# Kernel optimization log

Measured on AMD Instinct MI355X. Metric: run time of the kernel, lower is better.

## Reference

```python
import jax, jax.numpy as jnp
import numpy as np

N = 8192
D_IN, D_GAT, D_GCN = 128, 64, 64


def setup_inputs() -> dict:
    key = jax.random.key(0)
    ks = jax.random.split(key, 7)
    feat = jax.random.normal(ks[0], (N, D_IN), dtype=jnp.float32)
    r = jax.random.uniform(ks[1], (N, N), dtype=jnp.float32)
    sup = jnp.where(r < 0.01, r * 100.0, 0.0)
    xav = lambda k, shape: jax.random.normal(k, shape, dtype=jnp.float32) * jnp.sqrt(2.0 / (shape[0] + shape[1]))
    W_map = xav(ks[2], (D_IN, D_GAT))
    b_map = jnp.zeros((1,), dtype=jnp.float32)
    U = xav(ks[3], (D_GAT, 1))
    V = xav(ks[4], (D_GAT, 1))
    W_gcn = xav(ks[5], (D_GAT, D_GCN))
    return {"feat": feat, "sup": sup, "W_map": W_map, "b_map": b_map, "U": U, "V": V, "W_gcn": W_gcn}


def reference(feat, sup, W_map, b_map, U, V, W_gcn):
    n = sup.shape[0]
    sup2 = sup + jnp.eye(n, dtype=sup.dtype)  # add self-loops
    # GAT layer
    h = feat @ W_map                            # [N, D_GAT]
    s = h @ U                                   # [N, 1] score from source node i
    t = h @ V                                   # [N, 1] score from target node j
    # torch loop builds att[j, i] = tanh(s_i + t_j + b)
    att = jnp.tanh(s.T + t + b_map)             # [N, N]
    att = jnp.where(sup2 > 0, att, jnp.float32(-100.0))
    att = jax.nn.softmax(att, axis=1)
    gat_feat = jnp.tanh(att @ h)                # [N, D_GAT]
    # GCN layer (dropout is identity at inference)
    agg = sup2 @ gat_feat                       # [N, D_GAT]
    out = jax.nn.relu(agg @ W_gcn)              # [N, D_GCN]
    norm = jnp.linalg.norm(out, axis=1, keepdims=True)
    out = out / jnp.maximum(norm, jnp.float32(1e-12))  # F.normalize(p=2, dim=1)
    return out
```

## Files before the change

kernel.cpp:

```cpp
#include <hip/hip_runtime.h>
#include <hip/hip_bf16.h>


#define N_NODES 8192
#define D_IN    128
#define D_GAT   64
#define SLOTS   256

__global__ __launch_bounds__(256) void k1_map(
    const float* __restrict__ feat, const float* __restrict__ W_map,
    const float* __restrict__ U, const float* __restrict__ V,
    float* __restrict__ h, float* __restrict__ s, float* __restrict__ t)
{
    const int r = threadIdx.x >> 6;
    const int d = threadIdx.x & 63;
    const int row = blockIdx.x * 4 + r;
    __shared__ float f[4 * D_IN];
    if (threadIdx.x < 128)
        ((float4*)f)[threadIdx.x] =
            ((const float4*)(feat + (size_t)blockIdx.x * 4 * D_IN))[threadIdx.x];
    __syncthreads();

    const float* fr = f + r * D_IN;
    float acc = 0.f;
#pragma unroll 8
    for (int k = 0; k < D_IN; ++k)
        acc += fr[k] * W_map[k * D_GAT + d];
    h[row * D_GAT + d] = acc;

    float sv = acc * U[d];
    float tv = acc * V[d];
#pragma unroll
    for (int off = 32; off > 0; off >>= 1) {
        sv += __shfl_xor(sv, off);
        tv += __shfl_xor(tv, off);
    }
    if (d == 0) { s[row] = sv; t[row] = tv; }
}

__global__ __launch_bounds__(256) void k2_compact(
    const float* __restrict__ sup,
    int* __restrict__ cnt, int* __restrict__ col, float* __restrict__ val)
{
    const int j = blockIdx.x;
    const int lane = threadIdx.x & 63;
    __shared__ int c;
    if (threadIdx.x == 0) c = 0;
    __syncthreads();
    const float4* row = (const float4*)(sup + (size_t)j * N_NODES);
    int*   colj = col + j * SLOTS;
    float* valj = val + j * SLOTS;

    for (int q = threadIdx.x; q < N_NODES / 4; q += 256) {
        float4 v = row[q];
        const int i0 = q * 4;
        float vs[4] = {v.x, v.y, v.z, v.w};
#pragma unroll
        for (int u = 0; u < 4; ++u) {
            const int i = i0 + u;
            const float vv = vs[u] + ((i == j) ? 1.0f : 0.0f);
            const bool keep = vv > 0.f;
            const unsigned long long mask = __ballot(keep);
            if (mask) {
                int base = 0;
                if (lane == 0) base = atomicAdd(&c, __popcll(mask));
                base = __shfl(base, 0);
                if (keep) {
                    const int pos = base +
                        __popcll(mask & ((1ull << lane) - 1ull));
                    if (pos < SLOTS) { colj[pos] = i; valj[pos] = vv; }
                }
            }
        }
    }
    __syncthreads();
    if (threadIdx.x == 0) cnt[j] = (c < SLOTS) ? c : SLOTS;
}

__global__ __launch_bounds__(64) void k3_gat(
    const float* __restrict__ h, const float* __restrict__ s,
    const float* __restrict__ t, const float* __restrict__ b,
    const int* __restrict__ cnt, const int* __restrict__ col,
    float* __restrict__ gat)
{
    const int j = blockIdx.x;
    const int lane = threadIdx.x;
    const int m = cnt[j];
    const int* colj = col + j * SLOTS;
    __shared__ int   cl[SLOTS];
    __shared__ float w[SLOTS];
    const float tj = t[j] + b[0];

    float lmax = -1e30f;
    for (int p = lane; p < m; p += 64) {
        const int ci = colj[p];
        cl[p] = ci;
        const float e = tanhf(s[ci] + tj);
        w[p] = e;
        lmax = fmaxf(lmax, e);
    }
#pragma unroll
    for (int off = 32; off > 0; off >>= 1)
        lmax = fmaxf(lmax, __shfl_xor(lmax, off));

    float lsum = 0.f;
    for (int p = lane; p < m; p += 64) {
        const float e = __expf(w[p] - lmax);
        w[p] = e;
        lsum += e;
    }
#pragma unroll
    for (int off = 32; off > 0; off >>= 1) lsum += __shfl_xor(lsum, off);
    __syncthreads();

    const int c16 = (lane & 15) * 4;
    const int pp  = lane >> 4;
    float4 acc = make_float4(0.f, 0.f, 0.f, 0.f);
    for (int base = 0; base < m; base += 4) {
        const int p = base + pp;
        if (p < m) {
            const float wp = w[p];
            const float4 hv = *(const float4*)(h + cl[p] * D_GAT + c16);
            acc.x += wp * hv.x; acc.y += wp * hv.y;
            acc.z += wp * hv.z; acc.w += wp * hv.w;
        }
    }
#pragma unroll
    for (int off = 16; off <= 32; off <<= 1) {
        acc.x += __shfl_xor(acc.x, off); acc.y += __shfl_xor(acc.y, off);
        acc.z += __shfl_xor(acc.z, off); acc.w += __shfl_xor(acc.w, off);
    }
    if (pp == 0) {
        const float inv = 1.0f / lsum;
        float4 o;
        o.x = tanhf(acc.x * inv); o.y = tanhf(acc.y * inv);
        o.z = tanhf(acc.z * inv); o.w = tanhf(acc.w * inv);
        *(float4*)(gat + j * D_GAT + c16) = o;
    }
}

__global__ __launch_bounds__(64) void k4_gcn(
    const float* __restrict__ gat, const float* __restrict__ W_gcn,
    const int* __restrict__ cnt, const int* __restrict__ col,
    const float* __restrict__ val, float* __restrict__ out)
{
    const int j = blockIdx.x;
    const int lane = threadIdx.x;
    const int m = cnt[j];
    const int*   colj = col + j * SLOTS;
    const float* valj = val + j * SLOTS;
    __shared__ int   cl[SLOTS];
    __shared__ float wv[SLOTS];
    for (int p = lane; p < m; p += 64) { cl[p] = colj[p]; wv[p] = valj[p]; }
    __syncthreads();

    const int c16 = (lane & 15) * 4;
    const int pp  = lane >> 4;
    float4 acc = make_float4(0.f, 0.f, 0.f, 0.f);
    for (int base = 0; base < m; base += 4) {
        const int p = base + pp;
        if (p < m) {
            const float wp = wv[p];
            const float4 gv = *(const float4*)(gat + cl[p] * D_GAT + c16);
            acc.x += wp * gv.x; acc.y += wp * gv.y;
            acc.z += wp * gv.z; acc.w += wp * gv.w;
        }
    }
#pragma unroll
    for (int off = 16; off <= 32; off <<= 1) {
        acc.x += __shfl_xor(acc.x, off); acc.y += __shfl_xor(acc.y, off);
        acc.z += __shfl_xor(acc.z, off); acc.w += __shfl_xor(acc.w, off);
    }
    __shared__ float a[D_GAT];
    if (pp == 0) *(float4*)(a + c16) = acc;
    __syncthreads();

    float o = 0.f;
#pragma unroll 8
    for (int d = 0; d < D_GAT; ++d)
        o += a[d] * W_gcn[d * D_GAT + lane];
    o = fmaxf(o, 0.f);

    float ss = o * o;
#pragma unroll
    for (int off = 32; off > 0; off >>= 1) ss += __shfl_xor(ss, off);
    const float nrm = sqrtf(ss);
    out[j * D_GAT + lane] = o / fmaxf(nrm, 1e-12f);
}

extern "C" void kernel_launch(void* const* d_in, const int* in_sizes, int n_in,
                              void* d_out, int out_size, void* d_ws, size_t ws_size,
                              hipStream_t stream) {
    const float* feat  = (const float*)d_in[0];
    const float* sup   = (const float*)d_in[1];
    const float* W_map = (const float*)d_in[2];
    const float* b_map = (const float*)d_in[3];
    const float* U     = (const float*)d_in[4];
    const float* V     = (const float*)d_in[5];
    const float* W_gcn = (const float*)d_in[6];
    float* out = (float*)d_out;

    char* ws = (char*)d_ws;
    float* h   = (float*)(ws);
    float* gat = (float*)(ws + (2u << 20));
    float* s   = (float*)(ws + (4u << 20));
    float* t   = (float*)(ws + (4u << 20) + 32768);
    int*   cnt = (int*)  (ws + (4u << 20) + 65536);
    int*   col = (int*)  (ws + (4u << 20) + 98304);
    float* val = (float*)(ws + (12u << 20) + 98304);

    k1_map    <<<N_NODES / 4, 256, 0, stream>>>(feat, W_map, U, V, h, s, t);
    k2_compact<<<N_NODES,     256, 0, stream>>>(sup, cnt, col, val);
    k3_gat    <<<N_NODES,      64, 0, stream>>>(h, s, t, b_map, cnt, col, gat);
    k4_gcn    <<<N_NODES,      64, 0, stream>>>(gat, W_gcn, cnt, col, val, out);
}
```

Baseline: 412.1 us.

## Merge map and compaction kernels; pack four rows per block in gather kernels

Combines the feature-mapping kernel and the adjacency compaction kernel into a single launch, split by block index, which removes one launch and lets the two independent phases run concurrently. The GAT and GCN gather kernels now process four rows per 256-thread block, each wave using its own shared-memory slices. Their gather loops are unrolled by four with separate accumulators to keep more independent loads in flight. The total run is dominated by the compaction, which streams the dense 256 MB adjacency matrix, so these changes mostly trim overheads around that cost. Shared-memory use per block rises, and the block-wide barriers now couple four rows.

```diff
diff --git a/kernel.cpp b/kernel.cpp
--- a/kernel.cpp
+++ b/kernel.cpp
@@ -6,89 +6,89 @@
 #define D_IN    128
 #define D_GAT   64
 #define SLOTS   256
-
-__global__ __launch_bounds__(256) void k1_map(
+#define K1_BLOCKS (N_NODES / 4)
+
+__global__ __launch_bounds__(256) void k12_map_compact(
     const float* __restrict__ feat, const float* __restrict__ W_map,
     const float* __restrict__ U, const float* __restrict__ V,
-    float* __restrict__ h, float* __restrict__ s, float* __restrict__ t)
-{
-    const int r = threadIdx.x >> 6;
-    const int d = threadIdx.x & 63;
-    const int row = blockIdx.x * 4 + r;
-    __shared__ float f[4 * D_IN];
-    if (threadIdx.x < 128)
-        ((float4*)f)[threadIdx.x] =
-            ((const float4*)(feat + (size_t)blockIdx.x * 4 * D_IN))[threadIdx.x];
-    __syncthreads();
-
-    const float* fr = f + r * D_IN;
-    float acc = 0.f;
-#pragma unroll 8
-    for (int k = 0; k < D_IN; ++k)
-        acc += fr[k] * W_map[k * D_GAT + d];
-    h[row * D_GAT + d] = acc;
-
-    float sv = acc * U[d];
-    float tv = acc * V[d];
-#pragma unroll
-    for (int off = 32; off > 0; off >>= 1) {
-        sv += __shfl_xor(sv, off);
-        tv += __shfl_xor(tv, off);
-    }
-    if (d == 0) { s[row] = sv; t[row] = tv; }
-}
-
-__global__ __launch_bounds__(256) void k2_compact(
     const float* __restrict__ sup,
+    float* __restrict__ h, float* __restrict__ s, float* __restrict__ t,
     int* __restrict__ cnt, int* __restrict__ col, float* __restrict__ val)
 {
-    const int j = blockIdx.x;
-    const int lane = threadIdx.x & 63;
-    __shared__ int c;
-    if (threadIdx.x == 0) c = 0;
-    __syncthreads();
-    const float4* row = (const float4*)(sup + (size_t)j * N_NODES);
-    int*   colj = col + j * SLOTS;
-    float* valj = val + j * SLOTS;
-
-    for (int q = threadIdx.x; q < N_NODES / 4; q += 256) {
-        float4 v = row[q];
-        const int i0 = q * 4;
-        float vs[4] = {v.x, v.y, v.z, v.w};
-#pragma unroll
-        for (int u = 0; u < 4; ++u) {
-            const int i = i0 + u;
-            const float vv = vs[u] + ((i == j) ? 1.0f : 0.0f);
-            const bool keep = vv > 0.f;
-            const unsigned long long mask = __ballot(keep);
-            if (mask) {
-                int base = 0;
-                if (lane == 0) base = atomicAdd(&c, __popcll(mask));
-                base = __shfl(base, 0);
-                if (keep) {
-                    const int pos = base +
-                        __popcll(mask & ((1ull << lane) - 1ull));
-                    if (pos < SLOTS) { colj[pos] = i; valj[pos] = vv; }
+    if (blockIdx.x < K1_BLOCKS) {
+        const int r = threadIdx.x >> 6;
+        const int d = threadIdx.x & 63;
+        const int row = blockIdx.x * 4 + r;
+        __shared__ float f[4 * D_IN];
+        if (threadIdx.x < 128)
+            ((float4*)f)[threadIdx.x] =
+                ((const float4*)(feat + (size_t)blockIdx.x * 4 * D_IN))[threadIdx.x];
+        __syncthreads();
+        const float* fr = f + r * D_IN;
+        float acc = 0.f;
+#pragma unroll 8
+        for (int k = 0; k < D_IN; ++k)
+            acc += fr[k] * W_map[k * D_GAT + d];
+        h[row * D_GAT + d] = acc;
+        float sv = acc * U[d];
+        float tv = acc * V[d];
+#pragma unroll
+        for (int off = 32; off > 0; off >>= 1) {
+            sv += __shfl_xor(sv, off);
+            tv += __shfl_xor(tv, off);
+        }
+        if (d == 0) { s[row] = sv; t[row] = tv; }
+    } else {
+        const int j = blockIdx.x - K1_BLOCKS;
+        const int lane = threadIdx.x & 63;
+        __shared__ int c;
+        if (threadIdx.x == 0) c = 0;
+        __syncthreads();
+        const float4* row = (const float4*)(sup + (size_t)j * N_NODES);
+        int*   colj = col + j * SLOTS;
+        float* valj = val + j * SLOTS;
+        for (int q = threadIdx.x; q < N_NODES / 4; q += 256) {
+            float4 v = row[q];
+            const int i0 = q * 4;
+            float vs[4] = {v.x, v.y, v.z, v.w};
+#pragma unroll
+            for (int u = 0; u < 4; ++u) {
+                const int i = i0 + u;
+                const float vv = vs[u] + ((i == j) ? 1.0f : 0.0f);
+                const bool keep = vv > 0.f;
+                const unsigned long long mask = __ballot(keep);
+                if (mask) {
+                    int base = 0;
+                    if (lane == 0) base = atomicAdd(&c, __popcll(mask));
+                    base = __shfl(base, 0);
+                    if (keep) {
+                        const int pos = base +
+                            __popcll(mask & ((1ull << lane) - 1ull));
+                        if (pos < SLOTS) { colj[pos] = i; valj[pos] = vv; }
+                    }
                 }
             }
         }
-    }
-    __syncthreads();
-    if (threadIdx.x == 0) cnt[j] = (c < SLOTS) ? c : SLOTS;
-}
-
-__global__ __launch_bounds__(64) void k3_gat(
+        __syncthreads();
+        if (threadIdx.x == 0) cnt[j] = (c < SLOTS) ? c : SLOTS;
+    }
+}
+
+__global__ __launch_bounds__(256) void k3_gat(
     const float* __restrict__ h, const float* __restrict__ s,
     const float* __restrict__ t, const float* __restrict__ b,
     const int* __restrict__ cnt, const int* __restrict__ col,
     float* __restrict__ gat)
 {
-    const int j = blockIdx.x;
-    const int lane = threadIdx.x;
+    const int wid  = threadIdx.x >> 6;
+    const int lane = threadIdx.x & 63;
+    const int j = blockIdx.x * 4 + wid;
     const int m = cnt[j];
     const int* colj = col + j * SLOTS;
-    __shared__ int   cl[SLOTS];
-    __shared__ float w[SLOTS];
+    __shared__ int   cl_s[4][SLOTS];
+    __shared__ float w_s[4][SLOTS];
+    int*   cl = cl_s[wid];
+    float* w  = w_s[wid];
     const float tj = t[j] + b[0];
 
     float lmax = -1e30f;
@@ -115,16 +115,27 @@
 
     const int c16 = (lane & 15) * 4;
     const int pp  = lane >> 4;
-    float4 acc = make_float4(0.f, 0.f, 0.f, 0.f);
-    for (int base = 0; base < m; base += 4) {
-        const int p = base + pp;
-        if (p < m) {
-            const float wp = w[p];
-            const float4 hv = *(const float4*)(h + cl[p] * D_GAT + c16);
-            acc.x += wp * hv.x; acc.y += wp * hv.y;
-            acc.z += wp * hv.z; acc.w += wp * hv.w;
-        }
-    }
+    float4 a0 = make_float4(0,0,0,0), a1 = a0, a2 = a0, a3 = a0;
+    for (int base = 0; base < m; base += 16) {
+        const int p0 = base + pp, p1 = p0 + 4, p2 = p0 + 8, p3 = p0 + 12;
+        if (p0 < m) { const float wp = w[p0];
+            const float4 v = *(const float4*)(h + cl[p0] * D_GAT + c16);
+            a0.x += wp*v.x; a0.y += wp*v.y; a0.z += wp*v.z; a0.w += wp*v.w; }
+        if (p1 < m) { const float wp = w[p1];
+            const float4 v = *(const float4*)(h + cl[p1] * D_GAT + c16);
+            a1.x += wp*v.x; a1.y += wp*v.y; a1.z += wp*v.z; a1.w += wp*v.w; }
+        if (p2 < m) { const float wp = w[p2];
+            const float4 v = *(const float4*)(h + cl[p2] * D_GAT + c16);
+            a2.x += wp*v.x; a2.y += wp*v.y; a2.z += wp*v.z; a2.w += wp*v.w; }
+        if (p3 < m) { const float wp = w[p3];
+            const float4 v = *(const float4*)(h + cl[p3] * D_GAT + c16);
+            a3.x += wp*v.x; a3.y += wp*v.y; a3.z += wp*v.z; a3.w += wp*v.w; }
+    }
+    float4 acc;
+    acc.x = (a0.x + a1.x) + (a2.x + a3.x);
+    acc.y = (a0.y + a1.y) + (a2.y + a3.y);
+    acc.z = (a0.z + a1.z) + (a2.z + a3.z);
+    acc.w = (a0.w + a1.w) + (a2.w + a3.w);
 #pragma unroll
     for (int off = 16; off <= 32; off <<= 1) {
         acc.x += __shfl_xor(acc.x, off); acc.y += __shfl_xor(acc.y, off);
@@ -139,39 +150,54 @@
     }
 }
 
-__global__ __launch_bounds__(64) void k4_gcn(
+__global__ __launch_bounds__(256) void k4_gcn(
     const float* __restrict__ gat, const float* __restrict__ W_gcn,
     const int* __restrict__ cnt, const int* __restrict__ col,
     const float* __restrict__ val, float* __restrict__ out)
 {
-    const int j = blockIdx.x;
-    const int lane = threadIdx.x;
+    const int wid  = threadIdx.x >> 6;
+    const int lane = threadIdx.x & 63;
+    const int j = blockIdx.x * 4 + wid;
     const int m = cnt[j];
     const int*   colj = col + j * SLOTS;
     const float* valj = val + j * SLOTS;
-    __shared__ int   cl[SLOTS];
-    __shared__ float wv[SLOTS];
+    __shared__ int   cl_s[4][SLOTS];
+    __shared__ float wv_s[4][SLOTS];
+    __shared__ float a_s[4][D_GAT];
+    int*   cl = cl_s[wid];
+    float* wv = wv_s[wid];
+    float* a  = a_s[wid];
     for (int p = lane; p < m; p += 64) { cl[p] = colj[p]; wv[p] = valj[p]; }
     __syncthreads();
 
     const int c16 = (lane & 15) * 4;
     const int pp  = lane >> 4;
-    float4 acc = make_float4(0.f, 0.f, 0.f, 0.f);
-    for (int base = 0; base < m; base += 4) {
-        const int p = base + pp;
-        if (p < m) {
-            const float wp = wv[p];
-            const float4 gv = *(const float4*)(gat + cl[p] * D_GAT + c16);
-            acc.x += wp * gv.x; acc.y += wp * gv.y;
-            acc.z += wp * gv.z; acc.w += wp * gv.w;
-        }
-    }
+    float4 a0 = make_float4(0,0,0,0), a1 = a0, a2 = a0, a3 = a0;
+    for (int base = 0; base < m; base += 16) {
+        const int p0 = base + pp, p1 = p0 + 4, p2 = p0 + 8, p3 = p0 + 12;
+        if (p0 < m) { const float wp = wv[p0];
+            const float4 v = *(const float4*)(gat + cl[p0] * D_GAT + c16);
+            a0.x += wp*v.x; a0.y += wp*v.y; a0.z += wp*v.z; a0.w += wp*v.w; }
+        if (p1 < m) { const float wp = wv[p1];
+            const float4 v = *(const float4*)(gat + cl[p1] * D_GAT + c16);
+            a1.x += wp*v.x; a1.y += wp*v.y; a1.z += wp*v.z; a1.w += wp*v.w; }
+        if (p2 < m) { const float wp = wv[p2];
+            const float4 v = *(const float4*)(gat + cl[p2] * D_GAT + c16);
+            a2.x += wp*v.x; a2.y += wp*v.y; a2.z += wp*v.z; a2.w += wp*v.w; }
+        if (p3 < m) { const float wp = wv[p3];
+            const float4 v = *(const float4*)(gat + cl[p3] * D_GAT + c16);
+            a3.x += wp*v.x; a3.y += wp*v.y; a3.z += wp*v.z; a3.w += wp*v.w; }
+    }
+    float4 acc;
+    acc.x = (a0.x + a1.x) + (a2.x + a3.x);
+    acc.y = (a0.y + a1.y) + (a2.y + a3.y);
+    acc.z = (a0.z + a1.z) + (a2.z + a3.z);
+    acc.w = (a0.w + a1.w) + (a2.w + a3.w);
 #pragma unroll
     for (int off = 16; off <= 32; off <<= 1) {
         acc.x += __shfl_xor(acc.x, off); acc.y += __shfl_xor(acc.y, off);
         acc.z += __shfl_xor(acc.z, off); acc.w += __shfl_xor(acc.w, off);
     }
-    __shared__ float a[D_GAT];
     if (pp == 0) *(float4*)(a + c16) = acc;
     __syncthreads();
 
@@ -209,8 +235,8 @@
     int*   col = (int*)  (ws + (4u << 20) + 98304);
     float* val = (float*)(ws + (12u << 20) + 98304);
 
-    k1_map    <<<N_NODES / 4, 256, 0, stream>>>(feat, W_map, U, V, h, s, t);
-    k2_compact<<<N_NODES,     256, 0, stream>>>(sup, cnt, col, val);
-    k3_gat    <<<N_NODES,      64, 0, stream>>>(h, s, t, b_map, cnt, col, gat);
-    k4_gcn    <<<N_NODES,      64, 0, stream>>>(gat, W_gcn, cnt, col, val, out);
-}
+    k12_map_compact<<<K1_BLOCKS + N_NODES, 256, 0, stream>>>(
+        feat, W_map, U, V, sup, h, s, t, cnt, col, val);
+    k3_gat<<<N_NODES / 4, 256, 0, stream>>>(h, s, t, b_map, cnt, col, gat);
+    k4_gcn<<<N_NODES / 4, 256, 0, stream>>>(gat, W_gcn, cnt, col, val, out);
+}
```

Result: no change. 408.8 us (-0.8%).
